# Performance work log

Measured on AMD Instinct MI355X. Metric: run time of the kernel, lower is better.

## Reference

```python
import jax, jax.numpy as jnp
import numpy as np

NEG_INF = -jnp.inf


def _rope(x, cos, sin):
    # x: (B, S, H, D); cos/sin: (1, S, 1, D//2)
    xr = x.reshape(*x.shape[:-1], -1, 2)
    x1, x2 = xr[..., 0], xr[..., 1]  # (B, S, H, D//2) each
    # faithful to source: concat halves along last axis, same total size D
    return jnp.concatenate([x1 * cos - x2 * sin, x1 * sin + x2 * cos], axis=-1)


def setup_inputs() -> dict:
    B, S, D, H, Ld = 2, 2048, 2048, 16, 128
    key = jax.random.key(0)
    ks = jax.random.split(key, 6)
    sc = 1.0 / np.sqrt(D)
    return {
        "x": jax.random.normal(ks[0], (B, S, D), jnp.float32),
        "attn_mask": jnp.ones((B, S), jnp.int32),
        "Wq": jax.random.normal(ks[1], (D, H * Ld), jnp.float32) * sc,
        "bq": jnp.zeros((H * Ld,), jnp.float32),
        "Wk": jax.random.normal(ks[2], (D, H * Ld), jnp.float32) * sc,
        "bk": jnp.zeros((H * Ld,), jnp.float32),
        "Wv": jax.random.normal(ks[3], (D, H * Ld), jnp.float32) * sc,
        "bv": jnp.zeros((H * Ld,), jnp.float32),
        "Wo": jax.random.normal(ks[4], (H * Ld, D), jnp.float32) * sc,
        "bo": jnp.zeros((D,), jnp.float32),
        "num_heads": H,
    }


def reference(x, attn_mask, Wq, bq, Wk, bk, Wv, bv, Wo, bo, num_heads):
    B, S, D = x.shape
    H = int(num_heads)
    Ld = Wq.shape[1] // H
    base = 10000

    q = (x @ Wq + bq).reshape(B, S, H, Ld)
    k = (x @ Wk + bk).reshape(B, S, H, Ld)
    v = (x @ Wv + bv).reshape(B, S, H, Ld)

    # rotary tables (match RotaryEmbedding.setup, sliced to seq_len)
    inv_freq = 1.0 / base ** (2 * jnp.arange(0, Ld // 2) / Ld)
    angles = jnp.arange(S)[:, None] * inv_freq[None, :]  # (S, Ld//2)
    cos = jnp.cos(angles)[None, :, None, :].astype(x.dtype)
    sin = jnp.sin(angles)[None, :, None, :].astype(x.dtype)
    q = _rope(q, cos, sin)
    k = _rope(k, cos, sin)

    q = jnp.transpose(q, (0, 2, 1, 3))  # (B, H, S, Ld)
    k = jnp.transpose(k, (0, 2, 1, 3))
    v = jnp.transpose(v, (0, 2, 1, 3))

    scale = jnp.sqrt(jnp.float32(Ld)).astype(x.dtype)
    scores = jnp.einsum('bnqd,bnkd->bnqk', q, k) / scale  # (B, H, S, S)

    # faithful mask from source: keep where arange[None,:] >= arange[:,None]
    row_idx = jnp.arange(S)[None, :]
    col_idx = jnp.arange(S)[:, None]
    keep = row_idx >= col_idx  # (S, S)
    scores = jnp.where(keep[None, None, :, :], scores, NEG_INF)

    # padding mask applied over the QUERY axis, as in source: (B,1,S,1)
    scores = jnp.where(attn_mask[:, None, :, None] > 0, scores, NEG_INF)

    attn = jax.nn.softmax(scores, axis=-1)
    attended = jnp.einsum('bnqk,bnkd->bnqd', attn, v)
    attended = jnp.transpose(attended, (0, 2, 1, 3)).reshape(B, S, H * Ld)
    return attended @ Wo + bo
```

## Files before the change

kernel.cpp:

```cpp
#include <hip/hip_runtime.h>
#include <math.h>

typedef __bf16 bf16x8 __attribute__((ext_vector_type(8)));
typedef float f32x4 __attribute__((ext_vector_type(4)));

#define MFMA_BF16(a,b,c) __builtin_amdgcn_mfma_f32_16x16x32_bf16((a),(b),(c),0,0,0)

static constexpr int S_LEN = 2048;
static constexpr int DM    = 2048;
static constexpr int NHEAD = 16;
static constexpr int LDH   = 128;
static constexpr int BATCH = 2;
static constexpr size_t QKV_SEG = (size_t)BATCH * NHEAD * S_LEN * LDH;

__device__ __forceinline__ unsigned short f2bf(float f) {
    unsigned u = __float_as_uint(f);
    u += 0x7fffu + ((u >> 16) & 1u);
    return (unsigned short)(u >> 16);
}
__device__ __forceinline__ float bf2f(unsigned short h) {
    return __uint_as_float(((unsigned)h) << 16);
}
__device__ __forceinline__ float fexp2(float x) { return exp2f(x); }

__device__ __forceinline__ void ld_lds16(const void* g, void* l) {
    __builtin_amdgcn_global_load_lds(
        (const __attribute__((address_space(1))) unsigned int*)g,
        (__attribute__((address_space(3))) unsigned int*)l, 16, 0, 0);
}

__global__ void convert_f32_bf16(const float* __restrict__ in,
                                 unsigned short* __restrict__ out, int n4) {
    int idx = blockIdx.x * blockDim.x + threadIdx.x;
    if (idx >= n4) return;
    float4 v = reinterpret_cast<const float4*>(in)[idx];
    unsigned lo = (unsigned)f2bf(v.x) | ((unsigned)f2bf(v.y) << 16);
    unsigned hi = (unsigned)f2bf(v.z) | ((unsigned)f2bf(v.w) << 16);
    reinterpret_cast<uint2*>(out)[idx] = make_uint2(lo, hi);
}

__global__ void gen_tab(float* __restrict__ ct, float* __restrict__ st) {
    int i = threadIdx.x & 63;
    int s = blockIdx.x * 4 + (threadIdx.x >> 6);
    float freq = (float)exp(-(double)(2 * i) / 128.0 * 9.210340371976184);
    float a = (float)s * freq;
    ct[s * 64 + i] = cosf(a);
    st[s * 64 + i] = sinf(a);
}

__global__ void wconv_t4(const float* __restrict__ W0, const float* __restrict__ W1,
                         const float* __restrict__ W2, const float* __restrict__ W3,
                         unsigned short* __restrict__ O0, unsigned short* __restrict__ O1,
                         unsigned short* __restrict__ O2, unsigned short* __restrict__ O3) {
    __shared__ unsigned short tile[32][33];
    int z = blockIdx.z;
    const float* W = (z == 0) ? W0 : (z == 1) ? W1 : (z == 2) ? W2 : W3;
    unsigned short* Wt = (z == 0) ? O0 : (z == 1) ? O1 : (z == 2) ? O2 : O3;
    int n0 = blockIdx.x * 32;
    int k0 = blockIdx.y * 32;
    int t = threadIdx.x;
    int ir = t >> 3, ic = (t & 7) * 4;
    float4 v = *reinterpret_cast<const float4*>(&W[(size_t)(k0 + ir) * DM + n0 + ic]);
    tile[ir][ic + 0] = f2bf(v.x);
    tile[ir][ic + 1] = f2bf(v.y);
    tile[ir][ic + 2] = f2bf(v.z);
    tile[ir][ic + 3] = f2bf(v.w);
    __syncthreads();
    unsigned lo = (unsigned)tile[ic + 0][ir] | ((unsigned)tile[ic + 1][ir] << 16);
    unsigned hi = (unsigned)tile[ic + 2][ir] | ((unsigned)tile[ic + 3][ir] << 16);
    *reinterpret_cast<uint2*>(&Wt[(size_t)(n0 + ir) * DM + k0 + ic]) = make_uint2(lo, hi);
}

__global__ __launch_bounds__(256, 2) void gemm_bf16_out(
    const unsigned short* __restrict__ A,
    const unsigned short* __restrict__ Bt,
    const float* __restrict__ b0,
    float* __restrict__ outp)
{
    const int K = DM;
    __shared__ __attribute__((aligned(16))) unsigned short smem[8192];
    unsigned short* As = smem;
    unsigned short* Bs = smem + 4096;
    int t = threadIdx.x;
    int m0 = blockIdx.y * 128, n0 = blockIdx.x * 128;
    int lane = t & 63, i16 = lane & 15, quad = lane >> 4;
    int w = t >> 6;
    int wm = (w >> 1) * 64, wn = (w & 1) * 64;

    f32x4 acc[4][4];
    const f32x4 z4 = {0.f, 0.f, 0.f, 0.f};
    for (int mi = 0; mi < 4; ++mi)
        for (int ni = 0; ni < 4; ++ni) acc[mi][ni] = z4;

    for (int kk = 0; kk < K; kk += 32) {
        __syncthreads();
#pragma unroll
        for (int j = 0; j < 2; ++j) {
            int off = j * 4096 + w * 1024 + lane * 16;
            int row = off >> 6;
            int g = ((off >> 4) & 3) ^ ((row >> 1) & 3);
            ld_lds16(&A [(size_t)(m0 + row) * K + kk + g * 8], (char*)As + off);
            ld_lds16(&Bt[(size_t)(n0 + row) * K + kk + g * 8], (char*)Bs + off);
        }
        __syncthreads();

        bf16x8 aF[4], bF[4];
#pragma unroll
        for (int mi = 0; mi < 4; ++mi) {
            int rA = wm + mi * 16 + i16;
            aF[mi] = *reinterpret_cast<const bf16x8*>(
                (const char*)As + rA * 64 + ((quad ^ ((rA >> 1) & 3)) * 16));
        }
#pragma unroll
        for (int ni = 0; ni < 4; ++ni) {
            int rB = wn + ni * 16 + i16;
            bF[ni] = *reinterpret_cast<const bf16x8*>(
                (const char*)Bs + rB * 64 + ((quad ^ ((rB >> 1) & 3)) * 16));
        }
#pragma unroll
        for (int mi = 0; mi < 4; ++mi)
#pragma unroll
            for (int ni = 0; ni < 4; ++ni)
                acc[mi][ni] = MFMA_BF16(aF[mi], bF[ni], acc[mi][ni]);
    }

    for (int mi = 0; mi < 4; ++mi) {
        for (int ni = 0; ni < 4; ++ni) {
            int nn = n0 + wn + ni * 16 + i16;
            float bv = b0[nn];
            for (int r = 0; r < 4; ++r) {
                int mm = m0 + wm + mi * 16 + quad * 4 + r;
                outp[(size_t)mm * DM + nn] = acc[mi][ni][r] + bv;
            }
        }
    }
}

__global__ __launch_bounds__(512, 2) void gemm256_qkv(
    const unsigned short* __restrict__ A,
    const unsigned short* __restrict__ Bt,
    const float* __restrict__ b0, const float* __restrict__ b1,
    const float* __restrict__ b2,
    const float* __restrict__ ctab, const float* __restrict__ stab,
    unsigned short* __restrict__ outp)
{
    constexpr int K  = DM;
    constexpr int NT = K / 32;
    __shared__ __attribute__((aligned(16))) unsigned short smem[65536];

    int t = threadIdx.x, lane = t & 63, w = t >> 6;
    int i16 = lane & 15, quad = lane >> 4;
    int wc = w & 3, wr = w >> 2;

    int flat = blockIdx.y * 24 + blockIdx.x;
    int xcd = flat & 7, r8 = flat >> 3;
    int nbx = xcd * 3 + (r8 >> 4);
    int nby = r8 & 15;
    int m0 = nby * 256, n0 = nbx * 256;

    const unsigned short* ga[2];
    const unsigned short* gb[2];
    int loff[2];
#pragma unroll
    for (int j = 0; j < 2; ++j) {
        int off = j * 8192 + w * 1024 + lane * 16;
        int row = off >> 6;
        int q = ((off >> 4) & 3) ^ ((row >> 1) & 3);
        ga[j] = A  + (size_t)(m0 + row) * K + q * 8;
        gb[j] = Bt + (size_t)(n0 + row) * K + q * 8;
        loff[j] = off;
    }

    auto stage = [&](int slot, int kt) {
        char* base = (char*)smem + slot * 32768;
#pragma unroll
        for (int j = 0; j < 2; ++j) {
            ld_lds16(ga[j] + kt * 32, base + loff[j]);
            ld_lds16(gb[j] + kt * 32, base + 16384 + loff[j]);
        }
    };

    f32x4 acc[8][4];
    const f32x4 z4 = {0.f, 0.f, 0.f, 0.f};
#pragma unroll
    for (int mi = 0; mi < 8; ++mi)
#pragma unroll
        for (int ni = 0; ni < 4; ++ni) acc[mi][ni] = z4;

    auto compute = [&](int slot) {
        const char* Ab = (const char*)smem + slot * 32768;
        const char* Bb = Ab + 16384;
        bf16x8 bF[4];
#pragma unroll
        for (int ni = 0; ni < 4; ++ni) {
            int rB = wc * 64 + ni * 16 + i16;
            bF[ni] = *reinterpret_cast<const bf16x8*>(
                Bb + rB * 64 + ((quad ^ ((rB >> 1) & 3)) * 16));
        }
#pragma unroll
        for (int h = 0; h < 2; ++h) {
            bf16x8 aF[4];
#pragma unroll
            for (int mi = 0; mi < 4; ++mi) {
                int rA = wr * 128 + h * 64 + mi * 16 + i16;
                aF[mi] = *reinterpret_cast<const bf16x8*>(
                    Ab + rA * 64 + ((quad ^ ((rA >> 1) & 3)) * 16));
            }
            __builtin_amdgcn_s_setprio(1);
#pragma unroll
            for (int mi = 0; mi < 4; ++mi)
#pragma unroll
                for (int ni = 0; ni < 4; ++ni)
                    acc[h * 4 + mi][ni] = MFMA_BF16(aF[mi], bF[ni], acc[h * 4 + mi][ni]);
            __builtin_amdgcn_s_setprio(0);
        }
    };

    stage(0, 0); stage(1, 1); stage(2, 2);
    asm volatile("s_waitcnt vmcnt(8)" ::: "memory");
    __builtin_amdgcn_s_barrier();
    asm volatile("" ::: "memory");

    for (int tt = 0; tt < NT - 3; ++tt) {
        stage((tt + 3) & 3, tt + 3);
        compute(tt & 3);
        asm volatile("s_waitcnt vmcnt(8)" ::: "memory");
        __builtin_amdgcn_s_barrier();
        asm volatile("" ::: "memory");
    }
    compute((NT - 3) & 3);
    asm volatile("s_waitcnt vmcnt(4)" ::: "memory");
    __builtin_amdgcn_s_barrier();
    asm volatile("" ::: "memory");
    compute((NT - 2) & 3);
    asm volatile("s_waitcnt vmcnt(0)" ::: "memory");
    __builtin_amdgcn_s_barrier();
    asm volatile("" ::: "memory");
    compute((NT - 1) & 3);
    __syncthreads();

    unsigned short* Cs = smem;
    int which = n0 >> 11;
    int hh0 = (n0 & 2047) >> 7;
    const float* bp = (which == 0) ? b0 : ((which == 1) ? b1 : b2);
    int segn = n0 & 2047;
    int bb = m0 >> 11, s0 = m0 & 2047;

    if (which == 2) {
        int htile = wc >> 1;
#pragma unroll
        for (int mi = 0; mi < 8; ++mi)
#pragma unroll
            for (int ni = 0; ni < 4; ++ni) {
                int dcol = wc * 64 + ni * 16 + i16;
                int d = dcol & 127;
                float bv = bp[segn + dcol];
#pragma unroll
                for (int r = 0; r < 4; ++r) {
                    int sl = wr * 128 + mi * 16 + quad * 4 + r;
                    Cs[htile * 32768 + d * 256 + (((sl >> 3) ^ (d & 31)) * 8) + (sl & 7)] =
                        f2bf(acc[mi][ni][r] + bv);
                }
            }
        __syncthreads();
        unsigned short* vout = outp + 2 * QKV_SEG;
#pragma unroll
        for (int it = 0; it < 16; ++it) {
            int idx = it * 512 + t;
            int ht2 = idx >> 12, rem = idx & 4095, d = rem >> 5, sg = rem & 31;
            uint4 v = *reinterpret_cast<const uint4*>(
                &Cs[ht2 * 32768 + d * 256 + ((sg ^ (d & 31)) * 8)]);
            size_t oidx = (((size_t)(bb * NHEAD + hh0 + ht2)) * LDH + d) * S_LEN + s0 + sg * 8;
            *reinterpret_cast<uint4*>(vout + oidx) = v;
        }
    } else {
#pragma unroll
        for (int mi = 0; mi < 8; ++mi)
#pragma unroll
            for (int ni = 0; ni < 4; ++ni) {
                int nl = wc * 64 + ni * 16 + i16;
                float bv = bp[segn + nl];
#pragma unroll
                for (int r = 0; r < 4; ++r) {
                    int ml = wr * 128 + mi * 16 + quad * 4 + r;
                    Cs[ml * 256 + nl] = f2bf(acc[mi][ni][r] + bv);
                }
            }
        __syncthreads();
        float qscale = (which == 0) ? (0.08838834764831845f * 1.4426950408889634f) : 1.0f;
        unsigned short* qout = outp + (size_t)which * QKV_SEG;
#pragma unroll
        for (int it = 0; it < 16; ++it) {
            int idx = it * 512 + t;
            int row = idx >> 5, u = idx & 31, ht2 = u >> 4, c16 = u & 15;
            int mm = m0 + row, ss = mm & 2047, bb2 = mm >> 11;
            int i8 = (c16 & 7) * 8;
            const unsigned short* crow = Cs + row * 256 + ht2 * 128 + i8 * 2;
            uint4 w0 = *reinterpret_cast<const uint4*>(crow);
            uint4 w1 = *reinterpret_cast<const uint4*>(crow + 8);
            unsigned pw[8] = {w0.x, w0.y, w0.z, w0.w, w1.x, w1.y, w1.z, w1.w};
            float4 cA = *reinterpret_cast<const float4*>(&ctab[ss * 64 + i8]);
            float4 cB = *reinterpret_cast<const float4*>(&ctab[ss * 64 + i8 + 4]);
            float4 sA = *reinterpret_cast<const float4*>(&stab[ss * 64 + i8]);
            float4 sB = *reinterpret_cast<const float4*>(&stab[ss * 64 + i8 + 4]);
            float cv[8] = {cA.x, cA.y, cA.z, cA.w, cB.x, cB.y, cB.z, cB.w};
            float sv[8] = {sA.x, sA.y, sA.z, sA.w, sB.x, sB.y, sB.z, sB.w};
            bool hi = (c16 >= 8);
            unsigned short ov[8];
#pragma unroll
            for (int j = 0; j < 8; ++j) {
                float xe = bf2f((unsigned short)(pw[j] & 0xffff));
                float xo = bf2f((unsigned short)(pw[j] >> 16));
                float o = hi ? (xe * sv[j] + xo * cv[j]) : (xe * cv[j] - xo * sv[j]);
                ov[j] = f2bf(o * qscale);
            }
            size_t oidx = (((size_t)(bb2 * NHEAD + hh0 + ht2)) * S_LEN + ss) * LDH + c16 * 8;
            *reinterpret_cast<uint4*>(qout + oidx) =
                *reinterpret_cast<const uint4*>(ov);
        }
    }
}

__global__ __launch_bounds__(256, 2) void attn_kernel(
    const unsigned short* __restrict__ q,
    const unsigned short* __restrict__ k,
    const unsigned short* __restrict__ vt,
    unsigned short* __restrict__ att)
{
    __shared__ __attribute__((aligned(16))) unsigned short Ks[2][64 * 128];
    __shared__ __attribute__((aligned(16))) unsigned short Vs[2][128 * 64];
    __shared__ __attribute__((aligned(16))) unsigned short Ps[4][32 * 64];

    int bid = blockIdx.x;
    int second = bid >> 8;
    int p = bid & 255;
    int xb = second ? (15 - (p >> 5)) : (p >> 5);
    int bh = p & 31;
    int b = bh >> 4, h = bh & (NHEAD - 1);
    int q0 = xb * 128;

    int t = threadIdx.x, w = t >> 6, lane = t & 63;
    int i16 = lane & 15, quad = lane >> 4;
    int qbase = q0 + w * 32;

    bf16x8 qf[2][4];
#pragma unroll
    for (int qs = 0; qs < 2; ++qs) {
        const unsigned short* qrow = q + ((size_t)bh * S_LEN + qbase + qs * 16 + i16) * LDH;
#pragma unroll
        for (int c = 0; c < 4; ++c)
            qf[qs][c] = *reinterpret_cast<const bf16x8*>(qrow + c * 32 + quad * 8);
    }

    const f32x4 z4 = {0.f, 0.f, 0.f, 0.f};
    f32x4 o[2][8];
#pragma unroll
    for (int qs = 0; qs < 2; ++qs)
#pragma unroll
        for (int dt = 0; dt < 8; ++dt) o[qs][dt] = z4;
    float l_i[2] = {0.f, 0.f};

    const unsigned short* kbh  = k  + (size_t)bh * S_LEN * LDH;
    const unsigned short* vtbh = vt + (size_t)bh * LDH * S_LEN;
    unsigned short* PsW = Ps[w];

    auto stage = [&](int buf, int kk0) {
#pragma unroll
        for (int j = 0; j < 4; ++j) {
            int off = j * 4096 + w * 1024 + lane * 16;
            int key = off >> 8;
            int gk = ((off >> 4) & 15) ^ (key & 15);
            ld_lds16(&kbh[(size_t)(kk0 + key) * LDH + gk * 8], (char*)Ks[buf] + off);
            int d = off >> 7;
            int gv = ((off >> 4) & 7) ^ (d & 7);
            ld_lds16(&vtbh[(size_t)d * S_LEN + kk0 + gv * 8], (char*)Vs[buf] + off);
        }
    };

    stage(0, q0);
    int nch = (S_LEN - q0) >> 6;
    for (int ci = 0; ci < nch; ++ci) {
        __syncthreads();
        if (ci + 1 < nch) stage((ci + 1) & 1, q0 + (ci + 1) * 64);
        int kk0 = q0 + ci * 64;
        if (kk0 + 64 <= qbase) continue;
        const unsigned short* Kb = Ks[ci & 1];
        const unsigned short* Vb = Vs[ci & 1];

        f32x4 s[2][4];
#pragma unroll
        for (int qs = 0; qs < 2; ++qs)
#pragma unroll
            for (int kn = 0; kn < 4; ++kn) s[qs][kn] = z4;
#pragma unroll
        for (int c = 0; c < 4; ++c) {
            bf16x8 kf[4];
#pragma unroll
            for (int kn = 0; kn < 4; ++kn) {
                int key = kn * 16 + i16;
                int gs = (c * 4 + quad) ^ (key & 15);
                kf[kn] = *reinterpret_cast<const bf16x8*>((const char*)Kb + key * 256 + gs * 16);
            }
#pragma unroll
            for (int qs = 0; qs < 2; ++qs)
#pragma unroll
                for (int kn = 0; kn < 4; ++kn)
                    s[qs][kn] = MFMA_BF16(kf[kn], qf[qs][c], s[qs][kn]);
        }

        bool diag = (kk0 < qbase + 32);
#pragma unroll
        for (int qs = 0; qs < 2; ++qs) {
            int q_local = qs * 16 + i16;
            int qg = qbase + q_local;
#pragma unroll
            for (int kn = 0; kn < 4; ++kn) {
                int keyb = kk0 + kn * 16 + quad * 4;
                float pv[4];
                if (diag) {
#pragma unroll
                    for (int r = 0; r < 4; ++r)
                        pv[r] = (keyb + r >= qg) ? fexp2(s[qs][kn][r]) : 0.f;
                } else {
#pragma unroll
                    for (int r = 0; r < 4; ++r) pv[r] = fexp2(s[qs][kn][r]);
                }
                l_i[qs] += (pv[0] + pv[1]) + (pv[2] + pv[3]);
                unsigned lo = (unsigned)f2bf(pv[0]) | ((unsigned)f2bf(pv[1]) << 16);
                unsigned hi = (unsigned)f2bf(pv[2]) | ((unsigned)f2bf(pv[3]) << 16);
                int g = (kn * 2 + (quad >> 1)) ^ (q_local & 7);
                char* addr = (char*)PsW + q_local * 128 + g * 16 + (quad & 1) * 8;
                *reinterpret_cast<uint2*>(addr) = make_uint2(lo, hi);
            }
        }

#pragma unroll
        for (int hh = 0; hh < 2; ++hh) {
            bf16x8 pf[2];
#pragma unroll
            for (int qs = 0; qs < 2; ++qs) {
                int q_local = qs * 16 + i16;
                int g = (hh * 4 + quad) ^ (q_local & 7);
                pf[qs] = *reinterpret_cast<const bf16x8*>((const char*)PsW + q_local * 128 + g * 16);
            }
#pragma unroll
            for (int dt = 0; dt < 8; ++dt) {
                int d = dt * 16 + i16;
                int gv = (hh * 4 + quad) ^ (d & 7);
                bf16x8 vf = *reinterpret_cast<const bf16x8*>((const char*)Vb + d * 128 + gv * 16);
                o[0][dt] = MFMA_BF16(pf[0], vf, o[0][dt]);
                o[1][dt] = MFMA_BF16(pf[1], vf, o[1][dt]);
            }
        }
    }

#pragma unroll
    for (int qs = 0; qs < 2; ++qs) {
        float lr = l_i[qs];
        lr += __shfl_xor(lr, 16);
        lr += __shfl_xor(lr, 32);
        l_i[qs] = lr;
    }
#pragma unroll
    for (int qs = 0; qs < 2; ++qs) {
#pragma unroll
        for (int r = 0; r < 4; ++r) {
            float lv = __shfl(l_i[qs], quad * 4 + r);
            float inv = 1.0f / lv;
            int qrow = qbase + qs * 16 + quad * 4 + r;
            unsigned short* orow = att + ((size_t)b * S_LEN + qrow) * DM + h * LDH;
#pragma unroll
            for (int dt = 0; dt < 8; ++dt)
                orow[dt * 16 + i16] = f2bf(o[qs][dt][r] * inv);
        }
    }
}

extern "C" void kernel_launch(void* const* d_in, const int* in_sizes, int n_in,
                              void* d_out, int out_size, void* d_ws, size_t ws_size,
                              hipStream_t stream) {
    const float* x  = (const float*)d_in[0];
    const float* Wq = (const float*)d_in[2];
    const float* bq = (const float*)d_in[3];
    const float* Wk = (const float*)d_in[4];
    const float* bk = (const float*)d_in[5];
    const float* Wv = (const float*)d_in[6];
    const float* bv = (const float*)d_in[7];
    const float* Wo = (const float*)d_in[8];
    const float* bo = (const float*)d_in[9];

    char* ws = (char*)d_ws;
    unsigned short* xb  = (unsigned short*)(ws);
    unsigned short* Wqt = (unsigned short*)(ws + 16777216);
    unsigned short* Wkt = (unsigned short*)(ws + 25165824);
    unsigned short* Wvt = (unsigned short*)(ws + 33554432);
    unsigned short* Wot = (unsigned short*)(ws + 41943040);
    unsigned short* qkv = (unsigned short*)(ws + 50331648);
    unsigned short* att = (unsigned short*)(ws + 100663296);
    float* ctab = (float*)(ws + 117440512);
    float* stab = (float*)(ws + 117964800);

    convert_f32_bf16<<<8192, 256, 0, stream>>>(x, xb, (BATCH * S_LEN * DM) / 4);
    gen_tab<<<512, 256, 0, stream>>>(ctab, stab);
    wconv_t4<<<dim3(64, 64, 4), 256, 0, stream>>>(Wq, Wk, Wv, Wo, Wqt, Wkt, Wvt, Wot);

    gemm256_qkv<<<dim3(24, 16), 512, 0, stream>>>(
        xb, Wqt, bq, bk, bv, ctab, stab, qkv);

    attn_kernel<<<512, 256, 0, stream>>>(qkv, qkv + QKV_SEG, qkv + 2 * QKV_SEG, att);

    gemm_bf16_out<<<dim3(DM / 128, (BATCH * S_LEN) / 128), 256, 0, stream>>>(
        att, Wot, bo, (float*)d_out);
}
```

Baseline: 413.0 us.

## Shrink QKV GEMM tile to 256x128 with 4 waves and 3-stage pipeline

The QKV projection GEMM moves from a 256x256 tile with 512 threads and a 4-slot LDS ring to a 256x128 tile with 256 threads and a 3-slot ring. This doubles the grid to 768 blocks and cuts LDS per block from 128KB to 72KB, so more blocks can be resident per CU and load balance across CUs improves. The trade-off is less operand reuse per block (the A tile is re-read twice as often) and a shallower prefetch depth. The epilogue indexing is adjusted for one head per tile.

```diff
diff --git a/kernel.cpp b/kernel.cpp
--- a/kernel.cpp
+++ b/kernel.cpp
@@ -136,7 +136,7 @@
     }
 }
 
-__global__ __launch_bounds__(512, 2) void gemm256_qkv(
+__global__ __launch_bounds__(256, 2) void gemm_qkv_v2(
     const unsigned short* __restrict__ A,
     const unsigned short* __restrict__ Bt,
     const float* __restrict__ b0, const float* __restrict__ b1,
@@ -146,38 +146,47 @@
 {
     constexpr int K  = DM;
     constexpr int NT = K / 32;
-    __shared__ __attribute__((aligned(16))) unsigned short smem[65536];
+    constexpr int SLOT_B = 24576;
+    __shared__ __attribute__((aligned(16))) unsigned short smem[36864];
 
     int t = threadIdx.x, lane = t & 63, w = t >> 6;
     int i16 = lane & 15, quad = lane >> 4;
-    int wc = w & 3, wr = w >> 2;
-
-    int flat = blockIdx.y * 24 + blockIdx.x;
+    int wc = w & 1, wr = w >> 1;
+
+    int flat = blockIdx.y * 48 + blockIdx.x;
     int xcd = flat & 7, r8 = flat >> 3;
-    int nbx = xcd * 3 + (r8 >> 4);
+    int nbx = xcd * 6 + (r8 >> 4);
     int nby = r8 & 15;
-    int m0 = nby * 256, n0 = nbx * 256;
-
-    const unsigned short* ga[2];
+    int m0 = nby * 256, n0 = nbx * 128;
+
+    const unsigned short* ga[4];
     const unsigned short* gb[2];
-    int loff[2];
+    int loffA[4], loffB[2];
+#pragma unroll
+    for (int j = 0; j < 4; ++j) {
+        int off = j * 4096 + t * 16;
+        int row = off >> 6;
+        int g = ((off >> 4) & 3) ^ ((row >> 1) & 3);
+        ga[j] = A + (size_t)(m0 + row) * K + g * 8;
+        loffA[j] = off;
+    }
 #pragma unroll
     for (int j = 0; j < 2; ++j) {
-        int off = j * 8192 + w * 1024 + lane * 16;
+        int off = j * 4096 + t * 16;
         int row = off >> 6;
-        int q = ((off >> 4) & 3) ^ ((row >> 1) & 3);
-        ga[j] = A  + (size_t)(m0 + row) * K + q * 8;
-        gb[j] = Bt + (size_t)(n0 + row) * K + q * 8;
-        loff[j] = off;
+        int g = ((off >> 4) & 3) ^ ((row >> 1) & 3);
+        gb[j] = Bt + (size_t)(n0 + row) * K + g * 8;
+        loffB[j] = off;
     }
 
     auto stage = [&](int slot, int kt) {
-        char* base = (char*)smem + slot * 32768;
-#pragma unroll
-        for (int j = 0; j < 2; ++j) {
-            ld_lds16(ga[j] + kt * 32, base + loff[j]);
-            ld_lds16(gb[j] + kt * 32, base + 16384 + loff[j]);
-        }
+        char* base = (char*)smem + slot * SLOT_B;
+#pragma unroll
+        for (int j = 0; j < 4; ++j)
+            ld_lds16(ga[j] + kt * 32, base + loffA[j]);
+#pragma unroll
+        for (int j = 0; j < 2; ++j)
+            ld_lds16(gb[j] + kt * 32, base + 16384 + loffB[j]);
     };
 
     f32x4 acc[8][4];
@@ -188,7 +197,7 @@
         for (int ni = 0; ni < 4; ++ni) acc[mi][ni] = z4;
 
     auto compute = [&](int slot) {
-        const char* Ab = (const char*)smem + slot * 32768;
+        const char* Ab = (const char*)smem + slot * SLOT_B;
         const char* Bb = Ab + 16384;
         bf16x8 bF[4];
 #pragma unroll
@@ -216,49 +225,47 @@
         }
     };
 
-    stage(0, 0); stage(1, 1); stage(2, 2);
-    asm volatile("s_waitcnt vmcnt(8)" ::: "memory");
+    stage(0, 0); stage(1, 1);
+    asm volatile("s_waitcnt vmcnt(6)" ::: "memory");
     __builtin_amdgcn_s_barrier();
     asm volatile("" ::: "memory");
 
-    for (int tt = 0; tt < NT - 3; ++tt) {
-        stage((tt + 3) & 3, tt + 3);
-        compute(tt & 3);
-        asm volatile("s_waitcnt vmcnt(8)" ::: "memory");
+    int cs = 0, ssl = 2;
+    for (int tt = 0; tt < NT - 2; ++tt) {
+        stage(ssl, tt + 2);
+        compute(cs);
+        asm volatile("s_waitcnt vmcnt(6)" ::: "memory");
         __builtin_amdgcn_s_barrier();
         asm volatile("" ::: "memory");
-    }
-    compute((NT - 3) & 3);
-    asm volatile("s_waitcnt vmcnt(4)" ::: "memory");
-    __builtin_amdgcn_s_barrier();
-    asm volatile("" ::: "memory");
-    compute((NT - 2) & 3);
+        cs  = (cs  == 2) ? 0 : cs  + 1;
+        ssl = (ssl == 2) ? 0 : ssl + 1;
+    }
+    compute(cs);
     asm volatile("s_waitcnt vmcnt(0)" ::: "memory");
     __builtin_amdgcn_s_barrier();
     asm volatile("" ::: "memory");
-    compute((NT - 1) & 3);
+    cs = (cs == 2) ? 0 : cs + 1;
+    compute(cs);
     __syncthreads();
 
     unsigned short* Cs = smem;
     int which = n0 >> 11;
-    int hh0 = (n0 & 2047) >> 7;
+    int hh = (n0 & 2047) >> 7;
     const float* bp = (which == 0) ? b0 : ((which == 1) ? b1 : b2);
     int segn = n0 & 2047;
     int bb = m0 >> 11, s0 = m0 & 2047;
 
     if (which == 2) {
-        int htile = wc >> 1;
 #pragma unroll
         for (int mi = 0; mi < 8; ++mi)
 #pragma unroll
             for (int ni = 0; ni < 4; ++ni) {
-                int dcol = wc * 64 + ni * 16 + i16;
-                int d = dcol & 127;
-                float bv = bp[segn + dcol];
+                int d = wc * 64 + ni * 16 + i16;
+                float bv = bp[segn + d];
 #pragma unroll
                 for (int r = 0; r < 4; ++r) {
                     int sl = wr * 128 + mi * 16 + quad * 4 + r;
-                    Cs[htile * 32768 + d * 256 + (((sl >> 3) ^ (d & 31)) * 8) + (sl & 7)] =
+                    Cs[d * 256 + (((sl >> 3) ^ (d & 31)) * 8) + (sl & 7)] =
                         f2bf(acc[mi][ni][r] + bv);
                 }
             }
@@ -266,11 +273,11 @@
         unsigned short* vout = outp + 2 * QKV_SEG;
 #pragma unroll
         for (int it = 0; it < 16; ++it) {
-            int idx = it * 512 + t;
-            int ht2 = idx >> 12, rem = idx & 4095, d = rem >> 5, sg = rem & 31;
+            int idx = it * 256 + t;
+            int d = idx >> 5, sg = idx & 31;
             uint4 v = *reinterpret_cast<const uint4*>(
-                &Cs[ht2 * 32768 + d * 256 + ((sg ^ (d & 31)) * 8)]);
-            size_t oidx = (((size_t)(bb * NHEAD + hh0 + ht2)) * LDH + d) * S_LEN + s0 + sg * 8;
+                &Cs[d * 256 + ((sg ^ (d & 31)) * 8)]);
+            size_t oidx = (((size_t)(bb * NHEAD + hh)) * LDH + d) * S_LEN + s0 + sg * 8;
             *reinterpret_cast<uint4*>(vout + oidx) = v;
         }
     } else {
@@ -283,7 +290,7 @@
 #pragma unroll
                 for (int r = 0; r < 4; ++r) {
                     int ml = wr * 128 + mi * 16 + quad * 4 + r;
-                    Cs[ml * 256 + nl] = f2bf(acc[mi][ni][r] + bv);
+                    Cs[ml * 128 + nl] = f2bf(acc[mi][ni][r] + bv);
                 }
             }
         __syncthreads();
@@ -291,11 +298,12 @@
         unsigned short* qout = outp + (size_t)which * QKV_SEG;
 #pragma unroll
         for (int it = 0; it < 16; ++it) {
-            int idx = it * 512 + t;
-            int row = idx >> 5, u = idx & 31, ht2 = u >> 4, c16 = u & 15;
-            int mm = m0 + row, ss = mm & 2047, bb2 = mm >> 11;
+            int idx = it * 256 + t;
+            int row = idx >> 4, c16 = idx & 15;
+            int mm = m0 + row;
+            int ss = mm & 2047, bb2 = mm >> 11;
             int i8 = (c16 & 7) * 8;
-            const unsigned short* crow = Cs + row * 256 + ht2 * 128 + i8 * 2;
+            const unsigned short* crow = Cs + row * 128 + i8 * 2;
             uint4 w0 = *reinterpret_cast<const uint4*>(crow);
             uint4 w1 = *reinterpret_cast<const uint4*>(crow + 8);
             unsigned pw[8] = {w0.x, w0.y, w0.z, w0.w, w1.x, w1.y, w1.z, w1.w};
@@ -314,7 +322,7 @@
                 float o = hi ? (xe * sv[j] + xo * cv[j]) : (xe * cv[j] - xo * sv[j]);
                 ov[j] = f2bf(o * qscale);
             }
-            size_t oidx = (((size_t)(bb2 * NHEAD + hh0 + ht2)) * S_LEN + ss) * LDH + c16 * 8;
+            size_t oidx = (((size_t)(bb2 * NHEAD + hh)) * S_LEN + ss) * LDH + c16 * 8;
             *reinterpret_cast<uint4*>(qout + oidx) =
                 *reinterpret_cast<const uint4*>(ov);
         }
@@ -504,7 +512,7 @@
     gen_tab<<<512, 256, 0, stream>>>(ctab, stab);
     wconv_t4<<<dim3(64, 64, 4), 256, 0, stream>>>(Wq, Wk, Wv, Wo, Wqt, Wkt, Wvt, Wot);
 
-    gemm256_qkv<<<dim3(24, 16), 512, 0, stream>>>(
+    gemm_qkv_v2<<<dim3(48, 16), 256, 0, stream>>>(
         xb, Wqt, bq, bk, bv, ctab, stab, qkv);
 
     attn_kernel<<<512, 256, 0, stream>>>(qkv, qkv + QKV_SEG, qkv + 2 * QKV_SEG, att);
```

After: 396.0 us. -4.1%, faster.
